# Performance work log

Measured on AMD Instinct MI355X. Metric: run time of the kernel, lower is better.

## Reference

```python
import jax, jax.numpy as jnp
import numpy as np

SEQ, B, N = 128, 64, 128
IN_DIM, HID = 64, 128
K = 2          # max_diffusion_step
L = 2          # num_rnn_layers
M = K + 1      # num_matrices = n_supports*K + 1 (one 'laplacian' support)


def setup_inputs() -> dict:
    key = jax.random.key(0)
    ks = jax.random.split(key, 8)
    inputs = jax.random.normal(ks[0], (SEQ, B, N, IN_DIM), jnp.float32)
    initial_hidden_state = jnp.zeros((L, B, N * HID), jnp.float32)
    # scaled normalized-laplacian-like support; 1/N keeps chebyshev terms bounded
    supports = jax.random.normal(ks[1], (1, N, N), jnp.float32) / N

    def w(k, fan_in, out):
        return jax.random.normal(k, (fan_in, out), jnp.float32) / np.sqrt(fan_in).astype(np.float32)

    in0 = M * (IN_DIM + HID)   # layer 0 gconv input features (576)
    in1 = M * (HID + HID)      # layer 1 gconv input features (768)
    return {
        "inputs": inputs,
        "initial_hidden_state": initial_hidden_state,
        "supports": supports,
        "Wg0": w(ks[2], in0, 2 * HID), "bg0": jnp.zeros((2 * HID,), jnp.float32),
        "Wc0": w(ks[3], in0, HID),     "bc0": jnp.zeros((HID,), jnp.float32),
        "Wg1": w(ks[4], in1, 2 * HID), "bg1": jnp.zeros((2 * HID,), jnp.float32),
        "Wc1": w(ks[5], in1, HID),     "bc1": jnp.zeros((HID,), jnp.float32),
    }


def _gconv(x, support, W, b):
    # x: (B, N, F). Chebyshev diffusion: x0, x1=S@x0, x_k=2*S@x_{k-1}-x_{k-2}
    x0 = x
    x1 = jnp.einsum('mn,bnf->bmf', support, x0)
    mats = [x0, x1]
    for _ in range(2, K + 1):
        x2 = 2.0 * jnp.einsum('mn,bnf->bmf', support, x1) - x0
        mats.append(x2)
        x0, x1 = x1, x2
    xs = jnp.stack(mats, axis=-1)                 # (B, N, F, M) -- torch layout
    xs = xs.reshape(x.shape[0], x.shape[1], -1)   # (B, N, F*M)
    return xs @ W + b                             # (B, N, out)


def _dcgru_layer(x_seq, h0, support, Wg, bg, Wc, bc):
    # x_seq: (T, B, N, F); h0: (B, N, HID)
    def step(h, x_t):
        cat = jnp.concatenate([x_t, h], axis=-1)
        gates = jax.nn.sigmoid(_gconv(cat, support, Wg, bg))
        r, u = jnp.split(gates, 2, axis=-1)
        c = jnp.tanh(_gconv(jnp.concatenate([x_t, r * h], axis=-1), support, Wc, bc))
        h_new = u * h + (1.0 - u) * c
        return h_new, h_new
    return jax.lax.scan(step, h0, x_seq)


def reference(inputs, initial_hidden_state, supports, Wg0, bg0, Wc0, bc0, Wg1, bg1, Wc1, bc1):
    sup = supports[0]
    h0_0 = initial_hidden_state[0].reshape(B, N, HID)
    h0_1 = initial_hidden_state[1].reshape(B, N, HID)
    h_last0, ys0 = _dcgru_layer(inputs, h0_0, sup, Wg0, bg0, Wc0, bc0)
    h_last1, ys1 = _dcgru_layer(ys0, h0_1, sup, Wg1, bg1, Wc1, bc1)
    output_hidden = jnp.stack([h_last0, h_last1], axis=0).reshape(L, B, N * HID)
    outputs = ys1.reshape(SEQ, B, N * HID)
    return output_hidden, outputs
```

## Files before the change

kernel.cpp:

```cpp
#include <hip/hip_runtime.h>
#include <math.h>

#define SEQ 128
#define B 64
#define NN 128
#define IN_DIM 64
#define HID 128
#define BNH (B*NN*HID)

typedef unsigned short u16;
typedef __bf16 bf16x8 __attribute__((ext_vector_type(8)));
typedef float f32x4 __attribute__((ext_vector_type(4)));

__device__ __forceinline__ u16 f2bf(float f) {
    union { float f; unsigned u; } x; x.f = f;
    unsigned r = x.u + 0x7fffu + ((x.u >> 16) & 1u);
    return (u16)(r >> 16);
}
__device__ __forceinline__ float bf2f(u16 b) {
    union { unsigned u; float f; } x; x.u = ((unsigned)b) << 16; return x.f;
}
__device__ __forceinline__ bf16x8 ld_frag(const u16* p) {
    union { uint4 q; bf16x8 v; } u;
    u.q = *(const uint4*)p;
    return u.v;
}
__device__ __forceinline__ uint2 pack4(const f32x4& a) {
    uint2 pk;
    pk.x = (unsigned)f2bf(a[0]) | ((unsigned)f2bf(a[1]) << 16);
    pk.y = (unsigned)f2bf(a[2]) | ((unsigned)f2bf(a[3]) << 16);
    return pk;
}
__device__ __forceinline__ bf16x8 cvt8(const float* p) {
    float4 v0 = *(const float4*)p, v1 = *(const float4*)(p + 4);
    union { uint4 q; bf16x8 v; } t;
    t.q.x = (unsigned)f2bf(v0.x) | ((unsigned)f2bf(v0.y) << 16);
    t.q.y = (unsigned)f2bf(v0.z) | ((unsigned)f2bf(v0.w) << 16);
    t.q.z = (unsigned)f2bf(v1.x) | ((unsigned)f2bf(v1.y) << 16);
    t.q.w = (unsigned)f2bf(v1.z) | ((unsigned)f2bf(v1.w) << 16);
    return t.v;
}

__global__ void prep_A2_kernel(const float* __restrict__ S, u16* __restrict__ A2bf) {
    int idx = blockIdx.x * 256 + threadIdx.x;
    int m = idx >> 7, n = idx & 127;
    A2bf[idx] = f2bf(S[idx]);
    float acc = 0.f;
    #pragma unroll 4
    for (int k = 0; k < 128; ++k) acc += S[m*128 + k] * S[k*128 + n];
    A2bf[16384 + idx] = f2bf(2.f*acc - (m == n ? 1.f : 0.f));
}

__global__ void prep_A2f_kernel(const u16* __restrict__ A2bf, u16* __restrict__ A2f) {
    int idx = blockIdx.x * 256 + threadIdx.x;
    int j = idx & 7, lane = (idx >> 3) & 63, g = (idx >> 9) & 15, kc = idx >> 13;
    int mp = g*16 + (lane & 15);
    int n  = kc*32 + (lane >> 4)*8 + j;
    A2f[idx] = A2bf[mp*128 + n];
}

__global__ void prep_WTf_kernel(const float* __restrict__ W, u16* __restrict__ WTf,
                                int F, int NO) {
    int KK = 3 * F;
    int idx = blockIdx.x * 256 + threadIdx.x;
    if (idx >= NO * KK) return;
    int per = 512 * (NO/16);
    int kc = idx / per, rem = idx % per;
    int cg = rem >> 9, lane = (rem >> 3) & 63, j = idx & 7;
    int col = cg*16 + (lane & 15);
    int k = kc*32 + (lane >> 4)*8 + j;
    int m = k / F, f = k - m*F;
    WTf[idx] = f2bf(W[(size_t)(f*3 + m) * NO + col]);
}

__global__ void init_h_kernel(const float* __restrict__ h,
                              u16* __restrict__ hbf0, u16* __restrict__ h0T,
                              u16* __restrict__ hbf1, u16* __restrict__ h1T) {
    int i = blockIdx.x * 256 + threadIdx.x;
    int which = (i >= BNH);
    int j = which ? i - BNH : i;
    u16 v = f2bf(h[i]);
    int bn = j >> 7, col = j & 127;
    if (!which) { hbf0[j] = v; h0T[(size_t)col*8192 + bn] = v; }
    else        { hbf1[j] = v; h1T[(size_t)col*8192 + bn] = v; }
}

template<int L>
__device__ __forceinline__ void stepA(
    int b, int nh, int mh,
    const float* __restrict__ xf, const u16* __restrict__ hbX, const u16* __restrict__ xT,
    const u16* __restrict__ hbH, const u16* __restrict__ hTH,
    const u16* __restrict__ A2f, const u16* __restrict__ WTg, const float* __restrict__ bg,
    u16* __restrict__ rhb, u16* __restrict__ rhbT, float* __restrict__ ub,
    u16* __restrict__ xsgF, u16* smem)
{
    constexpr int FIN = L ? 128 : 64;
    constexpr int F   = L ? 256 : 192;
    constexpr int KK  = 3 * F;
    constexpr int FH  = F / 2;
    constexpr int NF2 = F / 32;
    const int tid = threadIdx.x;
    const int lane = tid & 63, w = tid >> 6;
    const int l15 = lane & 15, l16 = lane >> 4;

    if (L == 0) {
        for (int task = tid; task < 1024; task += 256) {
            int ng8 = task & 15, f = task >> 4, n0 = ng8*8, bn = b*NN + n0;
            union { uint4 q; u16 s[8]; } t;
            #pragma unroll
            for (int i = 0; i < 8; ++i) t.s[i] = f2bf(xf[(size_t)(bn + i)*IN_DIM + f]);
            *(uint4*)&smem[f*128 + (n0 ^ ((f & 7)*8))] = t.q;
        }
    }
    {
        const int R0 = L ? 0 : 64;
        const int NT = (F - R0) * 16;
        for (int task = tid; task < NT; task += 256) {
            int ng8 = task & 15, f = R0 + (task >> 4);
            const u16* src;
            if (L == 1) src = (f < 128) ? (xT + (size_t)f*8192) : (hTH + (size_t)(f - 128)*8192);
            else        src = hTH + (size_t)(f - 64)*8192;
            uint4 q = *(const uint4*)(src + (size_t)b*128 + ng8*8);
            *(uint4*)&smem[f*128 + ((ng8*8) ^ ((f & 7)*8))] = q;
        }
    }
    __syncthreads();

    const int mq = w;
    #pragma unroll
    for (int p = 0; p < 2; ++p) {
        const int fbase = (p == 0) ? FH : 0;
        f32x4 dacc[NF2][2];
        #pragma unroll
        for (int ff = 0; ff < NF2; ++ff)
            #pragma unroll
            for (int mm = 0; mm < 2; ++mm) dacc[ff][mm] = (f32x4)(0.f);
        #pragma unroll
        for (int kc = 0; kc < 4; ++kc) {
            bf16x8 bfr[2];
            #pragma unroll
            for (int mm = 0; mm < 2; ++mm) {
                const int g = (mq >> 1)*8 + mh*4 + (mq & 1)*2 + mm;
                bfr[mm] = ld_frag(A2f + (((size_t)kc*16 + g)*64 + lane)*8);
            }
            #pragma unroll
            for (int ff = 0; ff < NF2; ++ff) {
                const int f = fbase + ff*16 + l15;
                bf16x8 afr = ld_frag(&smem[f*128 + ((kc*32 + l16*8) ^ ((f & 7)*8))]);
                #pragma unroll
                for (int mm = 0; mm < 2; ++mm)
                    dacc[ff][mm] = __builtin_amdgcn_mfma_f32_16x16x32_bf16(afr, bfr[mm], dacc[ff][mm], 0, 0, 0);
            }
        }
        __syncthreads();
        const int fh = (p == 0) ? 1 : 0;
        #pragma unroll
        for (int ff = 0; ff < NF2; ++ff) {
            const int f4 = fbase + ff*16 + l16*4;
            const int col = f4 - fbase;
            #pragma unroll
            for (int mm = 0; mm < 2; ++mm) {
                const int r = mq*32 + mm*16 + l15;
                uint2 pk = pack4(dacc[ff][mm]);
                *(uint2*)&smem[fh*16384 + r*128 + (col ^ ((r & 7)*8))] = pk;
                if (nh == 0 && f4 < FIN) {
                    const int slot = r >> 6, node = mh*64 + (r & 63);
                    size_t off = ((((size_t)b*2 + slot)*(FIN/32) + (f4 >> 5))*8 + (node >> 4))*512
                               + (((f4 >> 3) & 3)*16 + (node & 15))*8 + (f4 & 7);
                    *(uint2*)(xsgF + off) = pk;
                }
            }
        }
    }
    __syncthreads();

    f32x4 pacc[4][2];
    #pragma unroll
    for (int fi = 0; fi < 4; ++fi)
        #pragma unroll
        for (int gj = 0; gj < 2; ++gj) pacc[fi][gj] = (f32x4)(0.f);

    #pragma unroll
    for (int kc = 0; kc < KK/32; ++kc) {
        const int k = kc*32, m = k / F, fIn = k - m*F;
        bf16x8 bb[2];
        #pragma unroll
        for (int gj = 0; gj < 2; ++gj) {
            const int cg = nh*8 + w*2 + gj;
            bb[gj] = ld_frag(WTg + (((size_t)kc*16 + cg)*64 + lane)*8);
        }
        #pragma unroll
        for (int fi = 0; fi < 4; ++fi) {
            const int node = mh*64 + fi*16 + l15;
            const int bn = b*NN + node;
            bf16x8 a;
            if (m == 0) {
                if (fIn < FIN) {
                    if (L == 0) a = cvt8(xf + (size_t)bn*IN_DIM + fIn + l16*8);
                    else        a = ld_frag(hbX + (size_t)bn*HID + fIn + l16*8);
                } else a = ld_frag(hbH + (size_t)bn*HID + (fIn - FIN) + l16*8);
            } else {
                const int r = (m - 1)*64 + fi*16 + l15;
                const int fh = (fIn >= FH) ? 1 : 0;
                const int col = fIn - fh*FH + l16*8;
                a = ld_frag(&smem[fh*16384 + r*128 + (col ^ ((r & 7)*8))]);
            }
            #pragma unroll
            for (int gj = 0; gj < 2; ++gj)
                pacc[fi][gj] = __builtin_amdgcn_mfma_f32_16x16x32_bf16(a, bb[gj], pacc[fi][gj], 0, 0, 0);
        }
    }
    #pragma unroll
    for (int fi = 0; fi < 4; ++fi) {
        const int node0 = mh*64 + fi*16 + l16*4;
        #pragma unroll
        for (int gj = 0; gj < 2; ++gj) {
            const int cl = (w*2 + gj)*16 + l15;
            if (nh == 0) {
                const float bcv = bg[cl];
                union { uint2 q; u16 s[4]; } pk;
                #pragma unroll
                for (int rr = 0; rr < 4; ++rr) {
                    const int bn = b*NN + node0 + rr;
                    const float v = pacc[fi][gj][rr] + bcv;
                    const float s = 1.f/(1.f + expf(-v));
                    const u16 rv = f2bf(s * bf2f(hbH[(size_t)bn*HID + cl]));
                    pk.s[rr] = rv;
                    rhb[(size_t)bn*HID + cl] = rv;
                }
                *(uint2*)&rhbT[(size_t)cl*8192 + (size_t)b*128 + node0] = pk.q;
            } else {
                const float bcv = bg[128 + cl];
                #pragma unroll
                for (int rr = 0; rr < 4; ++rr) {
                    const int bn = b*NN + node0 + rr;
                    const float v = pacc[fi][gj][rr] + bcv;
                    ub[(size_t)bn*HID + cl] = 1.f/(1.f + expf(-v));
                }
            }
        }
    }
}

template<int L>
__device__ __forceinline__ void stepB(
    int b, int mh,
    const float* __restrict__ xf, const u16* __restrict__ hbX,
    const u16* __restrict__ rhb, const u16* __restrict__ rhbT, const float* __restrict__ ub,
    const u16* __restrict__ xsgF, const u16* __restrict__ A2f,
    const u16* __restrict__ WTc, const float* __restrict__ bc,
    const float* __restrict__ hfR, float* __restrict__ hfW,
    u16* __restrict__ hbfW, u16* __restrict__ hTW,
    float* __restrict__ out2, u16* smem )
{
    constexpr int FIN = L ? 128 : 64;
    constexpr int F   = L ? 256 : 192;
    constexpr int KK  = 3 * F;
    const int tid = threadIdx.x;
    const int lane = tid & 63, w = tid >> 6;
    const int l15 = lane & 15, l16 = lane >> 4;

    f32x4 d2[4][2];
    #pragma unroll
    for (int ff = 0; ff < 4; ++ff)
        #pragma unroll
        for (int mm = 0; mm < 2; ++mm) d2[ff][mm] = (f32x4)(0.f);
    #pragma unroll
    for (int kc = 0; kc < 4; ++kc) {
        bf16x8 bfr[2];
        #pragma unroll
        for (int mm = 0; mm < 2; ++mm) {
            const int g = (w & 1)*8 + mh*2 + mm;
            bfr[mm] = ld_frag(A2f + (((size_t)kc*16 + g)*64 + lane)*8);
        }
        #pragma unroll
        for (int ff = 0; ff < 4; ++ff) {
            const int c = (w >> 1)*64 + ff*16 + l15;
            bf16x8 afr = ld_frag(rhbT + (size_t)c*8192 + (size_t)b*128 + kc*32 + l16*8);
            #pragma unroll
            for (int mm = 0; mm < 2; ++mm)
                d2[ff][mm] = __builtin_amdgcn_mfma_f32_16x16x32_bf16(afr, bfr[mm], d2[ff][mm], 0, 0, 0);
        }
    }
    #pragma unroll
    for (int ff = 0; ff < 4; ++ff) {
        const int c4 = (w >> 1)*64 + ff*16 + l16*4;
        #pragma unroll
        for (int mm = 0; mm < 2; ++mm) {
            const int r2 = (w & 1)*32 + mm*16 + l15;
            *(uint2*)&smem[r2*128 + (c4 ^ ((r2 & 7)*8))] = pack4(d2[ff][mm]);
        }
    }
    __syncthreads();

    f32x4 cacc[2][2];
    #pragma unroll
    for (int fi = 0; fi < 2; ++fi)
        #pragma unroll
        for (int gj = 0; gj < 2; ++gj) cacc[fi][gj] = (f32x4)(0.f);

    #pragma unroll
    for (int kc = 0; kc < KK/32; ++kc) {
        const int k = kc*32, m = k / F, fIn = k - m*F;
        bf16x8 bb[2];
        #pragma unroll
        for (int gj = 0; gj < 2; ++gj)
            bb[gj] = ld_frag(WTc + (((size_t)kc*8 + w*2 + gj)*64 + lane)*8);
        #pragma unroll
        for (int fi = 0; fi < 2; ++fi) {
            const int node = mh*32 + fi*16 + l15;
            const int bn = b*NN + node;
            bf16x8 a;
            if (m == 0) {
                if (fIn < FIN) {
                    if (L == 0) a = cvt8(xf + (size_t)bn*IN_DIM + fIn + l16*8);
                    else        a = ld_frag(hbX + (size_t)bn*HID + fIn + l16*8);
                } else a = ld_frag(rhb + (size_t)bn*HID + (fIn - FIN) + l16*8);
            } else if (fIn < FIN) {
                size_t off = ((((size_t)b*2 + (m - 1))*(FIN/32) + (fIn >> 5))*8 + (mh*2 + fi))*512
                           + (size_t)lane*8;
                a = ld_frag(xsgF + off);
            } else {
                const int r2 = (m - 1)*32 + fi*16 + l15;
                const int col = fIn - FIN + l16*8;
                a = ld_frag(&smem[r2*128 + (col ^ ((r2 & 7)*8))]);
            }
            #pragma unroll
            for (int gj = 0; gj < 2; ++gj)
                cacc[fi][gj] = __builtin_amdgcn_mfma_f32_16x16x32_bf16(a, bb[gj], cacc[fi][gj], 0, 0, 0);
        }
    }
    #pragma unroll
    for (int fi = 0; fi < 2; ++fi) {
        const int node0 = mh*32 + fi*16 + l16*4;
        #pragma unroll
        for (int gj = 0; gj < 2; ++gj) {
            const int cl = (w*2 + gj)*16 + l15;
            const float bcv = bc[cl];
            union { uint2 q; u16 s[4]; } pk;
            #pragma unroll
            for (int rr = 0; rr < 4; ++rr) {
                const int bn = b*NN + node0 + rr;
                const float v = cacc[fi][gj][rr] + bcv;
                const float cnd = tanhf(v);
                const float uu = ub[(size_t)bn*HID + cl];
                const float ho = hfR[(size_t)bn*HID + cl];
                const float hn = uu*ho + (1.f - uu)*cnd;
                hfW[(size_t)bn*HID + cl] = hn;
                const u16 hv = f2bf(hn);
                hbfW[(size_t)bn*HID + cl] = hv;
                pk.s[rr] = hv;
                if (L == 1) out2[(size_t)bn*HID + cl] = hn;
            }
            *(uint2*)&hTW[(size_t)cl*8192 + (size_t)b*128 + node0] = pk.q;
        }
    }
}

__global__ __launch_bounds__(256, 2) void kA(int zoff,
    const float* xf, const u16* A2f,
    const u16* hbf0r, const u16* h0Tr, const u16* hbf1r, const u16* h1Tr,
    const u16* WTgf0, const float* bg0, u16* rhb0, u16* rhbT0, float* ub0, u16* xsgF0,
    const u16* WTgf1, const float* bg1, u16* rhb1, u16* rhbT1, float* ub1, u16* xsgF1)
{
    extern __shared__ u16 smem[];
    const int b = blockIdx.x, nh = blockIdx.y >> 1, mh = blockIdx.y & 1;
    if ((int)blockIdx.z + zoff == 0)
        stepA<0>(b, nh, mh, xf, nullptr, nullptr, hbf0r, h0Tr, A2f,
                 WTgf0, bg0, rhb0, rhbT0, ub0, xsgF0, smem);
    else
        stepA<1>(b, nh, mh, nullptr, hbf0r, h0Tr, hbf1r, h1Tr, A2f,
                 WTgf1, bg1, rhb1, rhbT1, ub1, xsgF1, smem);
}

__global__ __launch_bounds__(256, 2) void kB(int zoff,
    const float* xf, const u16* A2f, const u16* hbf0r,
    const u16* rhb0, const u16* rhbT0, const float* ub0, const u16* xsgF0,
    const u16* WTcf0, const float* bc0,
    const float* hf0r, float* hf0w, u16* hbf0w, u16* h0Tw,
    const u16* rhb1, const u16* rhbT1, const float* ub1, const u16* xsgF1,
    const u16* WTcf1, const float* bc1,
    const float* hf1r, float* hf1w, u16* hbf1w, u16* h1Tw,
    float* out2)
{
    extern __shared__ u16 smem[];
    const int b = blockIdx.x, mh = blockIdx.y;
    if ((int)blockIdx.z + zoff == 0)
        stepB<0>(b, mh, xf, nullptr, rhb0, rhbT0, ub0, xsgF0, A2f, WTcf0, bc0,
                 hf0r, hf0w, hbf0w, h0Tw, nullptr, smem);
    else
        stepB<1>(b, mh, nullptr, hbf0r, rhb1, rhbT1, ub1, xsgF1, A2f, WTcf1, bc1,
                 hf1r, hf1w, hbf1w, h1Tw, out2, smem);
}

extern "C" void kernel_launch(void* const* d_in, const int* in_sizes, int n_in,
                              void* d_out, int out_size, void* d_ws, size_t ws_size,
                              hipStream_t stream) {
    (void)in_sizes; (void)n_in; (void)out_size; (void)ws_size;
    const float* inputs = (const float*)d_in[0];
    const float* h_init = (const float*)d_in[1];
    const float* S      = (const float*)d_in[2];
    const float* Wg0 = (const float*)d_in[3];
    const float* bg0 = (const float*)d_in[4];
    const float* Wc0 = (const float*)d_in[5];
    const float* bc0 = (const float*)d_in[6];
    const float* Wg1 = (const float*)d_in[7];
    const float* bg1 = (const float*)d_in[8];
    const float* Wc1 = (const float*)d_in[9];
    const float* bc1 = (const float*)d_in[10];

    float* out = (float*)d_out;
    float* outputs = out + 2 * (size_t)BNH;

    char* ws = (char*)d_ws;
    u16* A2bf  = (u16*)ws;                      ws += 32768 * 2;
    u16* A2f   = (u16*)ws;                      ws += 32768 * 2;
    u16* WTgf0 = (u16*)ws;                      ws += 256*576 * 2;
    u16* WTcf0 = (u16*)ws;                      ws += 128*576 * 2;
    u16* WTgf1 = (u16*)ws;                      ws += 256*768 * 2;
    u16* WTcf1 = (u16*)ws;                      ws += 128*768 * 2;
    ws = (char*)(((size_t)ws + 255) & ~(size_t)255);
    u16* xsgF0 = (u16*)ws;                      ws += (size_t)64*2*2*4096 * 2;
    u16* xsgF1 = (u16*)ws;                      ws += (size_t)64*2*4*4096 * 2;
    u16* rhb0  = (u16*)ws;                      ws += (size_t)BNH * 2;
    u16* rhb1  = (u16*)ws;                      ws += (size_t)BNH * 2;
    u16* rhbT0 = (u16*)ws;                      ws += (size_t)BNH * 2;
    u16* rhbT1 = (u16*)ws;                      ws += (size_t)BNH * 2;
    float* ub0 = (float*)ws;                    ws += (size_t)BNH * 4;
    float* ub1 = (float*)ws;                    ws += (size_t)BNH * 4;
    float* hf0_[2]; u16* hbf0_[2]; u16* h0T_[2];
    float* hf1_[2]; u16* hbf1_[2]; u16* h1T_[2];
    for (int i = 0; i < 2; ++i) {
        hf0_[i]  = (float*)ws;                  ws += (size_t)BNH * 4;
        hf1_[i]  = (float*)ws;                  ws += (size_t)BNH * 4;
        hbf0_[i] = (u16*)ws;                    ws += (size_t)BNH * 2;
        hbf1_[i] = (u16*)ws;                    ws += (size_t)BNH * 2;
        h0T_[i]  = (u16*)ws;                    ws += (size_t)BNH * 2;
        h1T_[i]  = (u16*)ws;                    ws += (size_t)BNH * 2;
    }

    hipFuncSetAttribute((const void*)kA, hipFuncAttributeMaxDynamicSharedMemorySize, 65536);
    hipFuncSetAttribute((const void*)kB, hipFuncAttributeMaxDynamicSharedMemorySize, 16384);

    hipMemcpyAsync(hf0_[1], h_init, (size_t)BNH * sizeof(float), hipMemcpyDeviceToDevice, stream);
    hipMemcpyAsync(hf1_[0], h_init + BNH, (size_t)BNH * sizeof(float), hipMemcpyDeviceToDevice, stream);
    init_h_kernel<<<(2*BNH + 255)/256, 256, 0, stream>>>(h_init, hbf0_[1], h0T_[1], hbf1_[0], h1T_[0]);
    prep_A2_kernel<<<64, 256, 0, stream>>>(S, A2bf);
    prep_A2f_kernel<<<128, 256, 0, stream>>>(A2bf, A2f);
    prep_WTf_kernel<<<(256*576 + 255)/256, 256, 0, stream>>>(Wg0, WTgf0, 192, 256);
    prep_WTf_kernel<<<(128*576 + 255)/256, 256, 0, stream>>>(Wc0, WTcf0, 192, 128);
    prep_WTf_kernel<<<(256*768 + 255)/256, 256, 0, stream>>>(Wg1, WTgf1, 256, 256);
    prep_WTf_kernel<<<(128*768 + 255)/256, 256, 0, stream>>>(Wc1, WTcf1, 256, 128);

    for (int tau = 0; tau <= SEQ; ++tau) {
        const int nz = (tau == 0 || tau == SEQ) ? 1 : 2;
        const int zoff = (tau == SEQ) ? 1 : 0;
        const int rb = (tau + 1) & 1, wb = tau & 1;
        const int tx = (tau < SEQ) ? tau : (SEQ - 1);
        const float* xt = inputs + (size_t)tx * B * NN * IN_DIM;
        float* out2 = outputs + (size_t)((tau > 0) ? tau - 1 : 0) * BNH;

        kA<<<dim3(64, 4, nz), 256, 65536, stream>>>(zoff,
            xt, A2f,
            hbf0_[rb], h0T_[rb], hbf1_[rb], h1T_[rb],
            WTgf0, bg0, rhb0, rhbT0, ub0, xsgF0,
            WTgf1, bg1, rhb1, rhbT1, ub1, xsgF1);
        kB<<<dim3(64, 4, nz), 256, 16384, stream>>>(zoff,
            xt, A2f, hbf0_[rb],
            rhb0, rhbT0, ub0, xsgF0, WTcf0, bc0,
            hf0_[rb], hf0_[wb], hbf0_[wb], h0T_[wb],
            rhb1, rhbT1, ub1, xsgF1, WTcf1, bc1,
            hf1_[rb], hf1_[wb], hbf1_[wb], h1T_[wb],
            out2);
    }
    hipMemcpyAsync(out, hf0_[1], (size_t)BNH * sizeof(float), hipMemcpyDeviceToDevice, stream);
    hipMemcpyAsync(out + BNH, hf1_[0], (size_t)BNH * sizeof(float), hipMemcpyDeviceToDevice, stream);
}
```

Measured before the change: 7.870 ms.

## Replace per-step kernel launches with persistent kernel and per-batch atomic barriers

The 258 small kernel launches (kA/kB per timestep) are replaced by a single persistent kernel of 512 blocks. Each batch element's 8 blocks (4 per layer) synchronise through a spin barrier on an atomic counter in global memory, and the barrier counter is zeroed in init_h_kernel. This removes launch overhead and grid-wide drains between stages, letting different batches progress independently. It relies on all 512 blocks being co-resident (2 per CU with 64KB LDS each) and risks deadlock or spin contention if that does not hold.

```diff
diff --git a/kernel.cpp b/kernel.cpp
--- a/kernel.cpp
+++ b/kernel.cpp
@@ -75,8 +75,10 @@
 
 __global__ void init_h_kernel(const float* __restrict__ h,
                               u16* __restrict__ hbf0, u16* __restrict__ h0T,
-                              u16* __restrict__ hbf1, u16* __restrict__ h1T) {
+                              u16* __restrict__ hbf1, u16* __restrict__ h1T,
+                              unsigned* __restrict__ bar) {
     int i = blockIdx.x * 256 + threadIdx.x;
+    if (blockIdx.x == 0 && threadIdx.x < 64) bar[threadIdx.x * 16] = 0;
     int which = (i >= BNH);
     int j = which ? i - BNH : i;
     u16 v = f2bf(h[i]);
@@ -357,40 +359,84 @@
     }
 }
 
-__global__ __launch_bounds__(256, 2) void kA(int zoff,
-    const float* xf, const u16* A2f,
-    const u16* hbf0r, const u16* h0Tr, const u16* hbf1r, const u16* h1Tr,
-    const u16* WTgf0, const float* bg0, u16* rhb0, u16* rhbT0, float* ub0, u16* xsgF0,
-    const u16* WTgf1, const float* bg1, u16* rhb1, u16* rhbT1, float* ub1, u16* xsgF1)
-{
+struct P {
+    const float* inputs; float* outputs;
+    const u16 *A2f, *WTg0, *WTc0, *WTg1, *WTc1;
+    const float *bg0, *bc0, *bg1, *bc1;
+    u16 *rhb0, *rhb1, *rhbT0, *rhbT1;
+    float *ub0, *ub1;
+    u16 *xsgF0, *xsgF1;
+    float *hf0_0, *hf0_1, *hf1_0, *hf1_1;
+    u16 *hbf0_0, *hbf0_1, *hbf1_0, *hbf1_1;
+    u16 *h0T_0, *h0T_1, *h1T_0, *h1T_1;
+    unsigned* bar;
+};
+
+__device__ __forceinline__ void bbar(unsigned* barw, unsigned tgt) {
+    __syncthreads();
+    if (threadIdx.x == 0) {
+        __hip_atomic_fetch_add(barw, 1u, __ATOMIC_RELEASE, __HIP_MEMORY_SCOPE_AGENT);
+        while (__hip_atomic_load(barw, __ATOMIC_ACQUIRE, __HIP_MEMORY_SCOPE_AGENT) < tgt)
+            __builtin_amdgcn_s_sleep(2);
+    }
+    __syncthreads();
+}
+
+template<int L>
+__device__ void run_chain(const P& p, int b, int quad, u16* smem) {
+    unsigned* barw = p.bar + b*16;
+    unsigned tgt = 0;
+    const int nh = quad >> 1, mh = quad & 1;
+    for (int iter = 0; iter <= SEQ; ++iter) {
+        const int rb = (iter + 1) & 1, wb = iter & 1;
+        const bool act = (L == 0) ? (iter < SEQ) : (iter >= 1);
+        const float* xf = p.inputs + (size_t)iter * (B*NN*IN_DIM);
+        const u16* hbf0r = rb ? p.hbf0_1 : p.hbf0_0;
+        const u16* h0Tr  = rb ? p.h0T_1  : p.h0T_0;
+
+        if (act) {
+            if (L == 0) {
+                stepA<0>(b, nh, mh, xf, nullptr, nullptr, hbf0r, h0Tr, p.A2f,
+                         p.WTg0, p.bg0, p.rhb0, p.rhbT0, p.ub0, p.xsgF0, smem);
+            } else {
+                const u16* hbf1r = rb ? p.hbf1_1 : p.hbf1_0;
+                const u16* h1Tr  = rb ? p.h1T_1  : p.h1T_0;
+                stepA<1>(b, nh, mh, nullptr, hbf0r, h0Tr, hbf1r, h1Tr, p.A2f,
+                         p.WTg1, p.bg1, p.rhb1, p.rhbT1, p.ub1, p.xsgF1, smem);
+            }
+        }
+        tgt += 8; bbar(barw, tgt);
+
+        if (act) {
+            if (L == 0) {
+                const float* hf0r = rb ? p.hf0_1 : p.hf0_0;
+                float* hf0w = wb ? p.hf0_1 : p.hf0_0;
+                u16* hbf0w = wb ? p.hbf0_1 : p.hbf0_0;
+                u16* h0Tw  = wb ? p.h0T_1  : p.h0T_0;
+                stepB<0>(b, quad, xf, nullptr, p.rhb0, p.rhbT0, p.ub0, p.xsgF0, p.A2f,
+                         p.WTc0, p.bc0, hf0r, hf0w, hbf0w, h0Tw, nullptr, smem);
+            } else {
+                const float* hf1r = rb ? p.hf1_1 : p.hf1_0;
+                float* hf1w = wb ? p.hf1_1 : p.hf1_0;
+                u16* hbf1w = wb ? p.hbf1_1 : p.hbf1_0;
+                u16* h1Tw  = wb ? p.h1T_1  : p.h1T_0;
+                float* out2 = p.outputs + (size_t)(iter - 1) * BNH;
+                stepB<1>(b, quad, nullptr, hbf0r, p.rhb1, p.rhbT1, p.ub1, p.xsgF1, p.A2f,
+                         p.WTc1, p.bc1, hf1r, hf1w, hbf1w, h1Tw, out2, smem);
+            }
+        }
+        tgt += 8; bbar(barw, tgt);
+    }
+}
+
+__global__ __launch_bounds__(256, 2) void kPersist(P p) {
     extern __shared__ u16 smem[];
-    const int b = blockIdx.x, nh = blockIdx.y >> 1, mh = blockIdx.y & 1;
-    if ((int)blockIdx.z + zoff == 0)
-        stepA<0>(b, nh, mh, xf, nullptr, nullptr, hbf0r, h0Tr, A2f,
-                 WTgf0, bg0, rhb0, rhbT0, ub0, xsgF0, smem);
-    else
-        stepA<1>(b, nh, mh, nullptr, hbf0r, h0Tr, hbf1r, h1Tr, A2f,
-                 WTgf1, bg1, rhb1, rhbT1, ub1, xsgF1, smem);
-}
-
-__global__ __launch_bounds__(256, 2) void kB(int zoff,
-    const float* xf, const u16* A2f, const u16* hbf0r,
-    const u16* rhb0, const u16* rhbT0, const float* ub0, const u16* xsgF0,
-    const u16* WTcf0, const float* bc0,
-    const float* hf0r, float* hf0w, u16* hbf0w, u16* h0Tw,
-    const u16* rhb1, const u16* rhbT1, const float* ub1, const u16* xsgF1,
-    const u16* WTcf1, const float* bc1,
-    const float* hf1r, float* hf1w, u16* hbf1w, u16* h1Tw,
-    float* out2)
-{
-    extern __shared__ u16 smem[];
-    const int b = blockIdx.x, mh = blockIdx.y;
-    if ((int)blockIdx.z + zoff == 0)
-        stepB<0>(b, mh, xf, nullptr, rhb0, rhbT0, ub0, xsgF0, A2f, WTcf0, bc0,
-                 hf0r, hf0w, hbf0w, h0Tw, nullptr, smem);
-    else
-        stepB<1>(b, mh, nullptr, hbf0r, rhb1, rhbT1, ub1, xsgF1, A2f, WTcf1, bc1,
-                 hf1r, hf1w, hbf1w, h1Tw, out2, smem);
+    const int bid = blockIdx.x;
+    const int b = bid & 63;
+    const int sub = bid >> 6;
+    const int L = sub >> 2, quad = sub & 3;
+    if (L == 0) run_chain<0>(p, b, quad, smem);
+    else        run_chain<1>(p, b, quad, smem);
 }
 
 extern "C" void kernel_launch(void* const* d_in, const int* in_sizes, int n_in,
@@ -419,6 +465,8 @@
     u16* WTcf0 = (u16*)ws;                      ws += 128*576 * 2;
     u16* WTgf1 = (u16*)ws;                      ws += 256*768 * 2;
     u16* WTcf1 = (u16*)ws;                      ws += 128*768 * 2;
+    ws = (char*)(((size_t)ws + 255) & ~(size_t)255);
+    unsigned* bar = (unsigned*)ws;              ws += 64*16*4;
     ws = (char*)(((size_t)ws + 255) & ~(size_t)255);
     u16* xsgF0 = (u16*)ws;                      ws += (size_t)64*2*2*4096 * 2;
     u16* xsgF1 = (u16*)ws;                      ws += (size_t)64*2*4*4096 * 2;
@@ -439,12 +487,11 @@
         h1T_[i]  = (u16*)ws;                    ws += (size_t)BNH * 2;
     }
 
-    hipFuncSetAttribute((const void*)kA, hipFuncAttributeMaxDynamicSharedMemorySize, 65536);
-    hipFuncSetAttribute((const void*)kB, hipFuncAttributeMaxDynamicSharedMemorySize, 16384);
+    hipFuncSetAttribute((const void*)kPersist, hipFuncAttributeMaxDynamicSharedMemorySize, 65536);
 
     hipMemcpyAsync(hf0_[1], h_init, (size_t)BNH * sizeof(float), hipMemcpyDeviceToDevice, stream);
     hipMemcpyAsync(hf1_[0], h_init + BNH, (size_t)BNH * sizeof(float), hipMemcpyDeviceToDevice, stream);
-    init_h_kernel<<<(2*BNH + 255)/256, 256, 0, stream>>>(h_init, hbf0_[1], h0T_[1], hbf1_[0], h1T_[0]);
+    init_h_kernel<<<(2*BNH + 255)/256, 256, 0, stream>>>(h_init, hbf0_[1], h0T_[1], hbf1_[0], h1T_[0], bar);
     prep_A2_kernel<<<64, 256, 0, stream>>>(S, A2bf);
     prep_A2f_kernel<<<128, 256, 0, stream>>>(A2bf, A2f);
     prep_WTf_kernel<<<(256*576 + 255)/256, 256, 0, stream>>>(Wg0, WTgf0, 192, 256);
@@ -452,27 +499,19 @@
     prep_WTf_kernel<<<(256*768 + 255)/256, 256, 0, stream>>>(Wg1, WTgf1, 256, 256);
     prep_WTf_kernel<<<(128*768 + 255)/256, 256, 0, stream>>>(Wc1, WTcf1, 256, 128);
 
-    for (int tau = 0; tau <= SEQ; ++tau) {
-        const int nz = (tau == 0 || tau == SEQ) ? 1 : 2;
-        const int zoff = (tau == SEQ) ? 1 : 0;
-        const int rb = (tau + 1) & 1, wb = tau & 1;
-        const int tx = (tau < SEQ) ? tau : (SEQ - 1);
-        const float* xt = inputs + (size_t)tx * B * NN * IN_DIM;
-        float* out2 = outputs + (size_t)((tau > 0) ? tau - 1 : 0) * BNH;
-
-        kA<<<dim3(64, 4, nz), 256, 65536, stream>>>(zoff,
-            xt, A2f,
-            hbf0_[rb], h0T_[rb], hbf1_[rb], h1T_[rb],
-            WTgf0, bg0, rhb0, rhbT0, ub0, xsgF0,
-            WTgf1, bg1, rhb1, rhbT1, ub1, xsgF1);
-        kB<<<dim3(64, 4, nz), 256, 16384, stream>>>(zoff,
-            xt, A2f, hbf0_[rb],
-            rhb0, rhbT0, ub0, xsgF0, WTcf0, bc0,
-            hf0_[rb], hf0_[wb], hbf0_[wb], h0T_[wb],
-            rhb1, rhbT1, ub1, xsgF1, WTcf1, bc1,
-            hf1_[rb], hf1_[wb], hbf1_[wb], h1T_[wb],
-            out2);
-    }
+    P p;
+    p.inputs = inputs; p.outputs = outputs;
+    p.A2f = A2f; p.WTg0 = WTgf0; p.WTc0 = WTcf0; p.WTg1 = WTgf1; p.WTc1 = WTcf1;
+    p.bg0 = bg0; p.bc0 = bc0; p.bg1 = bg1; p.bc1 = bc1;
+    p.rhb0 = rhb0; p.rhb1 = rhb1; p.rhbT0 = rhbT0; p.rhbT1 = rhbT1;
+    p.ub0 = ub0; p.ub1 = ub1; p.xsgF0 = xsgF0; p.xsgF1 = xsgF1;
+    p.hf0_0 = hf0_[0]; p.hf0_1 = hf0_[1]; p.hf1_0 = hf1_[0]; p.hf1_1 = hf1_[1];
+    p.hbf0_0 = hbf0_[0]; p.hbf0_1 = hbf0_[1]; p.hbf1_0 = hbf1_[0]; p.hbf1_1 = hbf1_[1];
+    p.h0T_0 = h0T_[0]; p.h0T_1 = h0T_[1]; p.h1T_0 = h1T_[0]; p.h1T_1 = h1T_[1];
+    p.bar = bar;
+
+    kPersist<<<512, 256, 65536, stream>>>(p);
+
     hipMemcpyAsync(out, hf0_[1], (size_t)BNH * sizeof(float), hipMemcpyDeviceToDevice, stream);
     hipMemcpyAsync(out + BNH, hf1_[0], (size_t)BNH * sizeof(float), hipMemcpyDeviceToDevice, stream);
 }
```

Measured after the change: 30.27 ms. 3.85x slower.

## Split DCGRU step kernels over finer node tiles and stage diffusion via global

Applied to the files above, without the earlier changes.

Both step kernels now launch 64x8 blocks instead of 64x4, and each block handles fewer nodes. Launch bounds move from 2 to 4 blocks per SM to raise occupancy. The shared-memory staging of inputs and hidden state in the gate kernel is removed: a one-time kernel pre-transposes all timesteps of the input to bf16, and diffusion results go to global scratch buffers that are read back after a block barrier. This removes large shared-memory use and boosts parallelism. The cost is duplicated diffusion work across nh blocks, extra global and L2 traffic, and a sizable extra workspace buffer.

```diff
diff --git a/kernel.cpp b/kernel.cpp
--- a/kernel.cpp
+++ b/kernel.cpp
@@ -73,6 +73,21 @@
     WTf[idx] = f2bf(W[(size_t)(f*3 + m) * NO + col]);
 }
 
+__global__ void prep_xT_kernel(const float* __restrict__ x, u16* __restrict__ xT) {
+    __shared__ u16 tile[64][72];
+    const int t = blockIdx.y, n0 = blockIdx.x * 64;
+    const int tid = threadIdx.x;
+    for (int i = tid; i < 4096; i += 256) {
+        int row = i >> 6, f = i & 63;
+        tile[f][row] = f2bf(x[((size_t)t*8192 + n0 + row)*64 + f]);
+    }
+    __syncthreads();
+    for (int i = tid; i < 4096; i += 256) {
+        int f = i >> 6, col = i & 63;
+        xT[((size_t)t*64 + f)*8192 + n0 + col] = tile[f][col];
+    }
+}
+
 __global__ void init_h_kernel(const float* __restrict__ h,
                               u16* __restrict__ hbf0, u16* __restrict__ h0T,
                               u16* __restrict__ hbf1, u16* __restrict__ h1T) {
@@ -88,11 +103,14 @@
 template<int L>
 __device__ __forceinline__ void stepA(
     int b, int nh, int mh,
-    const float* __restrict__ xf, const u16* __restrict__ hbX, const u16* __restrict__ xT,
-    const u16* __restrict__ hbH, const u16* __restrict__ hTH,
+    const float* __restrict__ xf,
+    const u16* __restrict__ xTt,
+    const u16* __restrict__ hbX,
+    const u16* __restrict__ hbH,
+    const u16* __restrict__ hTH,
     const u16* __restrict__ A2f, const u16* __restrict__ WTg, const float* __restrict__ bg,
     u16* __restrict__ rhb, u16* __restrict__ rhbT, float* __restrict__ ub,
-    u16* __restrict__ xsgF, u16* smem)
+    u16* __restrict__ Dg)
 {
     constexpr int FIN = L ? 128 : 64;
     constexpr int F   = L ? 256 : 192;
@@ -103,80 +121,44 @@
     const int lane = tid & 63, w = tid >> 6;
     const int l15 = lane & 15, l16 = lane >> 4;
 
-    if (L == 0) {
-        for (int task = tid; task < 1024; task += 256) {
-            int ng8 = task & 15, f = task >> 4, n0 = ng8*8, bn = b*NN + n0;
-            union { uint4 q; u16 s[8]; } t;
-            #pragma unroll
-            for (int i = 0; i < 8; ++i) t.s[i] = f2bf(xf[(size_t)(bn + i)*IN_DIM + f]);
-            *(uint4*)&smem[f*128 + (n0 ^ ((f & 7)*8))] = t.q;
-        }
-    }
-    {
-        const int R0 = L ? 0 : 64;
-        const int NT = (F - R0) * 16;
-        for (int task = tid; task < NT; task += 256) {
-            int ng8 = task & 15, f = R0 + (task >> 4);
-            const u16* src;
-            if (L == 1) src = (f < 128) ? (xT + (size_t)f*8192) : (hTH + (size_t)(f - 128)*8192);
-            else        src = hTH + (size_t)(f - 64)*8192;
-            uint4 q = *(const uint4*)(src + (size_t)b*128 + ng8*8);
-            *(uint4*)&smem[f*128 + ((ng8*8) ^ ((f & 7)*8))] = q;
-        }
-    }
-    __syncthreads();
-
-    const int mq = w;
+    const int g     = (w >> 1)*8 + mh*2 + (w & 1);
+    const int slot  = w >> 1;
+    const int nodeg = mh*2 + (w & 1);
     #pragma unroll
     for (int p = 0; p < 2; ++p) {
-        const int fbase = (p == 0) ? FH : 0;
-        f32x4 dacc[NF2][2];
-        #pragma unroll
-        for (int ff = 0; ff < NF2; ++ff)
-            #pragma unroll
-            for (int mm = 0; mm < 2; ++mm) dacc[ff][mm] = (f32x4)(0.f);
+        const int fbase = p ? FH : 0;
+        f32x4 dacc[NF2];
+        #pragma unroll
+        for (int ff = 0; ff < NF2; ++ff) dacc[ff] = (f32x4)(0.f);
         #pragma unroll
         for (int kc = 0; kc < 4; ++kc) {
-            bf16x8 bfr[2];
-            #pragma unroll
-            for (int mm = 0; mm < 2; ++mm) {
-                const int g = (mq >> 1)*8 + mh*4 + (mq & 1)*2 + mm;
-                bfr[mm] = ld_frag(A2f + (((size_t)kc*16 + g)*64 + lane)*8);
-            }
+            bf16x8 bfr = ld_frag(A2f + (((size_t)kc*16 + g)*64 + lane)*8);
             #pragma unroll
             for (int ff = 0; ff < NF2; ++ff) {
-                const int f = fbase + ff*16 + l15;
-                bf16x8 afr = ld_frag(&smem[f*128 + ((kc*32 + l16*8) ^ ((f & 7)*8))]);
-                #pragma unroll
-                for (int mm = 0; mm < 2; ++mm)
-                    dacc[ff][mm] = __builtin_amdgcn_mfma_f32_16x16x32_bf16(afr, bfr[mm], dacc[ff][mm], 0, 0, 0);
+                const int fr = fbase + ff*16;
+                const int f  = fr + l15;
+                const u16* src;
+                if (L == 1) src = (fr < 128) ? (xTt + (size_t)f*8192)
+                                             : (hTH + (size_t)(f - 128)*8192);
+                else        src = (fr < 64)  ? (xTt + (size_t)f*8192)
+                                             : (hTH + (size_t)(f - 64)*8192);
+                bf16x8 afr = ld_frag(src + (size_t)b*128 + kc*32 + l16*8);
+                dacc[ff] = __builtin_amdgcn_mfma_f32_16x16x32_bf16(afr, bfr, dacc[ff], 0, 0, 0);
             }
         }
-        __syncthreads();
-        const int fh = (p == 0) ? 1 : 0;
         #pragma unroll
         for (int ff = 0; ff < NF2; ++ff) {
             const int f4 = fbase + ff*16 + l16*4;
-            const int col = f4 - fbase;
-            #pragma unroll
-            for (int mm = 0; mm < 2; ++mm) {
-                const int r = mq*32 + mm*16 + l15;
-                uint2 pk = pack4(dacc[ff][mm]);
-                *(uint2*)&smem[fh*16384 + r*128 + (col ^ ((r & 7)*8))] = pk;
-                if (nh == 0 && f4 < FIN) {
-                    const int slot = r >> 6, node = mh*64 + (r & 63);
-                    size_t off = ((((size_t)b*2 + slot)*(FIN/32) + (f4 >> 5))*8 + (node >> 4))*512
-                               + (((f4 >> 3) & 3)*16 + (node & 15))*8 + (f4 & 7);
-                    *(uint2*)(xsgF + off) = pk;
-                }
-            }
+            size_t off = (((size_t)(b*2 + slot)*(F/32) + (f4 >> 5))*8 + nodeg)*512
+                       + (((f4 >> 3) & 3)*16 + l15)*8 + (f4 & 7);
+            *(uint2*)(Dg + off) = pack4(dacc[ff]);
         }
     }
     __syncthreads();
 
-    f32x4 pacc[4][2];
-    #pragma unroll
-    for (int fi = 0; fi < 4; ++fi)
+    f32x4 pacc[2][2];
+    #pragma unroll
+    for (int fi = 0; fi < 2; ++fi)
         #pragma unroll
         for (int gj = 0; gj < 2; ++gj) pacc[fi][gj] = (f32x4)(0.f);
 
@@ -190,8 +172,8 @@
             bb[gj] = ld_frag(WTg + (((size_t)kc*16 + cg)*64 + lane)*8);
         }
         #pragma unroll
-        for (int fi = 0; fi < 4; ++fi) {
-            const int node = mh*64 + fi*16 + l15;
+        for (int fi = 0; fi < 2; ++fi) {
+            const int node = mh*32 + fi*16 + l15;
             const int bn = b*NN + node;
             bf16x8 a;
             if (m == 0) {
@@ -200,10 +182,9 @@
                     else        a = ld_frag(hbX + (size_t)bn*HID + fIn + l16*8);
                 } else a = ld_frag(hbH + (size_t)bn*HID + (fIn - FIN) + l16*8);
             } else {
-                const int r = (m - 1)*64 + fi*16 + l15;
-                const int fh = (fIn >= FH) ? 1 : 0;
-                const int col = fIn - fh*FH + l16*8;
-                a = ld_frag(&smem[fh*16384 + r*128 + (col ^ ((r & 7)*8))]);
+                size_t off = (((size_t)(b*2 + (m-1))*(F/32) + (fIn >> 5))*8 + (mh*2 + fi))*512
+                           + (size_t)lane*8;
+                a = ld_frag(Dg + off);
             }
             #pragma unroll
             for (int gj = 0; gj < 2; ++gj)
@@ -211,8 +192,8 @@
         }
     }
     #pragma unroll
-    for (int fi = 0; fi < 4; ++fi) {
-        const int node0 = mh*64 + fi*16 + l16*4;
+    for (int fi = 0; fi < 2; ++fi) {
+        const int node0 = mh*32 + fi*16 + l16*4;
         #pragma unroll
         for (int gj = 0; gj < 2; ++gj) {
             const int cl = (w*2 + gj)*16 + l15;
@@ -247,7 +228,7 @@
     int b, int mh,
     const float* __restrict__ xf, const u16* __restrict__ hbX,
     const u16* __restrict__ rhb, const u16* __restrict__ rhbT, const float* __restrict__ ub,
-    const u16* __restrict__ xsgF, const u16* __restrict__ A2f,
+    const u16* __restrict__ Dg0, const u16* __restrict__ A2f,
     const u16* __restrict__ WTc, const float* __restrict__ bc,
     const float* __restrict__ hfR, float* __restrict__ hfW,
     u16* __restrict__ hbfW, u16* __restrict__ hTW,
@@ -260,44 +241,40 @@
     const int lane = tid & 63, w = tid >> 6;
     const int l15 = lane & 15, l16 = lane >> 4;
 
-    f32x4 d2[4][2];
-    #pragma unroll
-    for (int ff = 0; ff < 4; ++ff)
-        #pragma unroll
-        for (int mm = 0; mm < 2; ++mm) d2[ff][mm] = (f32x4)(0.f);
+    f32x4 d2[2][2];
+    #pragma unroll
+    for (int cc = 0; cc < 2; ++cc)
+        #pragma unroll
+        for (int mm = 0; mm < 2; ++mm) d2[cc][mm] = (f32x4)(0.f);
     #pragma unroll
     for (int kc = 0; kc < 4; ++kc) {
         bf16x8 bfr[2];
         #pragma unroll
-        for (int mm = 0; mm < 2; ++mm) {
-            const int g = (w & 1)*8 + mh*2 + mm;
-            bfr[mm] = ld_frag(A2f + (((size_t)kc*16 + g)*64 + lane)*8);
-        }
-        #pragma unroll
-        for (int ff = 0; ff < 4; ++ff) {
-            const int c = (w >> 1)*64 + ff*16 + l15;
+        for (int mm = 0; mm < 2; ++mm)
+            bfr[mm] = ld_frag(A2f + (((size_t)kc*16 + mm*8 + mh)*64 + lane)*8);
+        #pragma unroll
+        for (int cc = 0; cc < 2; ++cc) {
+            const int c = (w*2 + cc)*16 + l15;
             bf16x8 afr = ld_frag(rhbT + (size_t)c*8192 + (size_t)b*128 + kc*32 + l16*8);
             #pragma unroll
             for (int mm = 0; mm < 2; ++mm)
-                d2[ff][mm] = __builtin_amdgcn_mfma_f32_16x16x32_bf16(afr, bfr[mm], d2[ff][mm], 0, 0, 0);
-        }
-    }
-    #pragma unroll
-    for (int ff = 0; ff < 4; ++ff) {
-        const int c4 = (w >> 1)*64 + ff*16 + l16*4;
+                d2[cc][mm] = __builtin_amdgcn_mfma_f32_16x16x32_bf16(afr, bfr[mm], d2[cc][mm], 0, 0, 0);
+        }
+    }
+    #pragma unroll
+    for (int cc = 0; cc < 2; ++cc) {
+        const int c4 = (w*2 + cc)*16 + l16*4;
         #pragma unroll
         for (int mm = 0; mm < 2; ++mm) {
-            const int r2 = (w & 1)*32 + mm*16 + l15;
-            *(uint2*)&smem[r2*128 + (c4 ^ ((r2 & 7)*8))] = pack4(d2[ff][mm]);
+            const int r2 = mm*16 + l15;
+            *(uint2*)&smem[r2*128 + (c4 ^ ((r2 & 7)*8))] = pack4(d2[cc][mm]);
         }
     }
     __syncthreads();
 
-    f32x4 cacc[2][2];
-    #pragma unroll
-    for (int fi = 0; fi < 2; ++fi)
-        #pragma unroll
-        for (int gj = 0; gj < 2; ++gj) cacc[fi][gj] = (f32x4)(0.f);
+    f32x4 cacc[2];
+    #pragma unroll
+    for (int gj = 0; gj < 2; ++gj) cacc[gj] = (f32x4)(0.f);
 
     #pragma unroll
     for (int kc = 0; kc < KK/32; ++kc) {
@@ -306,90 +283,83 @@
         #pragma unroll
         for (int gj = 0; gj < 2; ++gj)
             bb[gj] = ld_frag(WTc + (((size_t)kc*8 + w*2 + gj)*64 + lane)*8);
-        #pragma unroll
-        for (int fi = 0; fi < 2; ++fi) {
-            const int node = mh*32 + fi*16 + l15;
-            const int bn = b*NN + node;
-            bf16x8 a;
-            if (m == 0) {
-                if (fIn < FIN) {
-                    if (L == 0) a = cvt8(xf + (size_t)bn*IN_DIM + fIn + l16*8);
-                    else        a = ld_frag(hbX + (size_t)bn*HID + fIn + l16*8);
-                } else a = ld_frag(rhb + (size_t)bn*HID + (fIn - FIN) + l16*8);
-            } else if (fIn < FIN) {
-                size_t off = ((((size_t)b*2 + (m - 1))*(FIN/32) + (fIn >> 5))*8 + (mh*2 + fi))*512
-                           + (size_t)lane*8;
-                a = ld_frag(xsgF + off);
-            } else {
-                const int r2 = (m - 1)*32 + fi*16 + l15;
-                const int col = fIn - FIN + l16*8;
-                a = ld_frag(&smem[r2*128 + (col ^ ((r2 & 7)*8))]);
-            }
-            #pragma unroll
-            for (int gj = 0; gj < 2; ++gj)
-                cacc[fi][gj] = __builtin_amdgcn_mfma_f32_16x16x32_bf16(a, bb[gj], cacc[fi][gj], 0, 0, 0);
-        }
-    }
-    #pragma unroll
-    for (int fi = 0; fi < 2; ++fi) {
-        const int node0 = mh*32 + fi*16 + l16*4;
-        #pragma unroll
-        for (int gj = 0; gj < 2; ++gj) {
-            const int cl = (w*2 + gj)*16 + l15;
-            const float bcv = bc[cl];
-            union { uint2 q; u16 s[4]; } pk;
-            #pragma unroll
-            for (int rr = 0; rr < 4; ++rr) {
-                const int bn = b*NN + node0 + rr;
-                const float v = cacc[fi][gj][rr] + bcv;
-                const float cnd = tanhf(v);
-                const float uu = ub[(size_t)bn*HID + cl];
-                const float ho = hfR[(size_t)bn*HID + cl];
-                const float hn = uu*ho + (1.f - uu)*cnd;
-                hfW[(size_t)bn*HID + cl] = hn;
-                const u16 hv = f2bf(hn);
-                hbfW[(size_t)bn*HID + cl] = hv;
-                pk.s[rr] = hv;
-                if (L == 1) out2[(size_t)bn*HID + cl] = hn;
-            }
-            *(uint2*)&hTW[(size_t)cl*8192 + (size_t)b*128 + node0] = pk.q;
-        }
-    }
-}
-
-__global__ __launch_bounds__(256, 2) void kA(int zoff,
-    const float* xf, const u16* A2f,
+        const int node = mh*16 + l15;
+        const int bn = b*NN + node;
+        bf16x8 a;
+        if (m == 0) {
+            if (fIn < FIN) {
+                if (L == 0) a = cvt8(xf + (size_t)bn*IN_DIM + fIn + l16*8);
+                else        a = ld_frag(hbX + (size_t)bn*HID + fIn + l16*8);
+            } else a = ld_frag(rhb + (size_t)bn*HID + (fIn - FIN) + l16*8);
+        } else if (fIn < FIN) {
+            size_t off = (((size_t)(b*2 + (m-1))*(F/32) + (fIn >> 5))*8 + mh)*512
+                       + (size_t)lane*8;
+            a = ld_frag(Dg0 + off);
+        } else {
+            const int r2 = (m-1)*16 + l15;
+            a = ld_frag(&smem[r2*128 + (((fIn - FIN) + l16*8) ^ ((r2 & 7)*8))]);
+        }
+        #pragma unroll
+        for (int gj = 0; gj < 2; ++gj)
+            cacc[gj] = __builtin_amdgcn_mfma_f32_16x16x32_bf16(a, bb[gj], cacc[gj], 0, 0, 0);
+    }
+    const int node0 = mh*16 + l16*4;
+    #pragma unroll
+    for (int gj = 0; gj < 2; ++gj) {
+        const int cl = (w*2 + gj)*16 + l15;
+        const float bcv = bc[cl];
+        union { uint2 q; u16 s[4]; } pk;
+        #pragma unroll
+        for (int rr = 0; rr < 4; ++rr) {
+            const int bn = b*NN + node0 + rr;
+            const float v = cacc[gj][rr] + bcv;
+            const float cnd = tanhf(v);
+            const float uu = ub[(size_t)bn*HID + cl];
+            const float ho = hfR[(size_t)bn*HID + cl];
+            const float hn = uu*ho + (1.f - uu)*cnd;
+            hfW[(size_t)bn*HID + cl] = hn;
+            const u16 hv = f2bf(hn);
+            hbfW[(size_t)bn*HID + cl] = hv;
+            pk.s[rr] = hv;
+            if (L == 1) out2[(size_t)bn*HID + cl] = hn;
+        }
+        *(uint2*)&hTW[(size_t)cl*8192 + (size_t)b*128 + node0] = pk.q;
+    }
+}
+
+__global__ __launch_bounds__(256, 4) void kA(int zoff,
+    const float* xf, const u16* xTt, const u16* A2f,
     const u16* hbf0r, const u16* h0Tr, const u16* hbf1r, const u16* h1Tr,
-    const u16* WTgf0, const float* bg0, u16* rhb0, u16* rhbT0, float* ub0, u16* xsgF0,
-    const u16* WTgf1, const float* bg1, u16* rhb1, u16* rhbT1, float* ub1, u16* xsgF1)
+    const u16* WTgf0, const float* bg0, u16* rhb0, u16* rhbT0, float* ub0, u16* Dg00, u16* Dg01,
+    const u16* WTgf1, const float* bg1, u16* rhb1, u16* rhbT1, float* ub1, u16* Dg10, u16* Dg11)
 {
-    extern __shared__ u16 smem[];
-    const int b = blockIdx.x, nh = blockIdx.y >> 1, mh = blockIdx.y & 1;
+    const int b = blockIdx.x, y = blockIdx.y;
+    const int nh = y >> 2, mh = y & 3;
     if ((int)blockIdx.z + zoff == 0)
-        stepA<0>(b, nh, mh, xf, nullptr, nullptr, hbf0r, h0Tr, A2f,
-                 WTgf0, bg0, rhb0, rhbT0, ub0, xsgF0, smem);
+        stepA<0>(b, nh, mh, xf, xTt, nullptr, hbf0r, h0Tr, A2f, WTgf0, bg0,
+                 rhb0, rhbT0, ub0, nh ? Dg01 : Dg00);
     else
-        stepA<1>(b, nh, mh, nullptr, hbf0r, h0Tr, hbf1r, h1Tr, A2f,
-                 WTgf1, bg1, rhb1, rhbT1, ub1, xsgF1, smem);
-}
-
-__global__ __launch_bounds__(256, 2) void kB(int zoff,
+        stepA<1>(b, nh, mh, nullptr, h0Tr, hbf0r, hbf1r, h1Tr, A2f, WTgf1, bg1,
+                 rhb1, rhbT1, ub1, nh ? Dg11 : Dg10);
+}
+
+__global__ __launch_bounds__(256, 4) void kB(int zoff,
     const float* xf, const u16* A2f, const u16* hbf0r,
-    const u16* rhb0, const u16* rhbT0, const float* ub0, const u16* xsgF0,
+    const u16* rhb0, const u16* rhbT0, const float* ub0, const u16* Dg00,
     const u16* WTcf0, const float* bc0,
     const float* hf0r, float* hf0w, u16* hbf0w, u16* h0Tw,
-    const u16* rhb1, const u16* rhbT1, const float* ub1, const u16* xsgF1,
+    const u16* rhb1, const u16* rhbT1, const float* ub1, const u16* Dg10,
     const u16* WTcf1, const float* bc1,
     const float* hf1r, float* hf1w, u16* hbf1w, u16* h1Tw,
     float* out2)
 {
-    extern __shared__ u16 smem[];
+    __shared__ u16 smem[32*128];
     const int b = blockIdx.x, mh = blockIdx.y;
     if ((int)blockIdx.z + zoff == 0)
-        stepB<0>(b, mh, xf, nullptr, rhb0, rhbT0, ub0, xsgF0, A2f, WTcf0, bc0,
+        stepB<0>(b, mh, xf, nullptr, rhb0, rhbT0, ub0, Dg00, A2f, WTcf0, bc0,
                  hf0r, hf0w, hbf0w, h0Tw, nullptr, smem);
     else
-        stepB<1>(b, mh, nullptr, hbf0r, rhb1, rhbT1, ub1, xsgF1, A2f, WTcf1, bc1,
+        stepB<1>(b, mh, nullptr, hbf0r, rhb1, rhbT1, ub1, Dg10, A2f, WTcf1, bc1,
                  hf1r, hf1w, hbf1w, h1Tw, out2, smem);
 }
 
@@ -420,8 +390,11 @@
     u16* WTgf1 = (u16*)ws;                      ws += 256*768 * 2;
     u16* WTcf1 = (u16*)ws;                      ws += 128*768 * 2;
     ws = (char*)(((size_t)ws + 255) & ~(size_t)255);
-    u16* xsgF0 = (u16*)ws;                      ws += (size_t)64*2*2*4096 * 2;
-    u16* xsgF1 = (u16*)ws;                      ws += (size_t)64*2*4*4096 * 2;
+    u16* xTall = (u16*)ws;                      ws += (size_t)SEQ*64*8192 * 2;
+    u16* Dg00  = (u16*)ws;                      ws += (size_t)128*6*8*512 * 2;
+    u16* Dg01  = (u16*)ws;                      ws += (size_t)128*6*8*512 * 2;
+    u16* Dg10  = (u16*)ws;                      ws += (size_t)128*8*8*512 * 2;
+    u16* Dg11  = (u16*)ws;                      ws += (size_t)128*8*8*512 * 2;
     u16* rhb0  = (u16*)ws;                      ws += (size_t)BNH * 2;
     u16* rhb1  = (u16*)ws;                      ws += (size_t)BNH * 2;
     u16* rhbT0 = (u16*)ws;                      ws += (size_t)BNH * 2;
@@ -439,9 +412,6 @@
         h1T_[i]  = (u16*)ws;                    ws += (size_t)BNH * 2;
     }
 
-    hipFuncSetAttribute((const void*)kA, hipFuncAttributeMaxDynamicSharedMemorySize, 65536);
-    hipFuncSetAttribute((const void*)kB, hipFuncAttributeMaxDynamicSharedMemorySize, 16384);
-
     hipMemcpyAsync(hf0_[1], h_init, (size_t)BNH * sizeof(float), hipMemcpyDeviceToDevice, stream);
     hipMemcpyAsync(hf1_[0], h_init + BNH, (size_t)BNH * sizeof(float), hipMemcpyDeviceToDevice, stream);
     init_h_kernel<<<(2*BNH + 255)/256, 256, 0, stream>>>(h_init, hbf0_[1], h0T_[1], hbf1_[0], h1T_[0]);
@@ -451,6 +421,7 @@
     prep_WTf_kernel<<<(128*576 + 255)/256, 256, 0, stream>>>(Wc0, WTcf0, 192, 128);
     prep_WTf_kernel<<<(256*768 + 255)/256, 256, 0, stream>>>(Wg1, WTgf1, 256, 256);
     prep_WTf_kernel<<<(128*768 + 255)/256, 256, 0, stream>>>(Wc1, WTcf1, 256, 128);
+    prep_xT_kernel<<<dim3(128, SEQ), 256, 0, stream>>>(inputs, xTall);
 
     for (int tau = 0; tau <= SEQ; ++tau) {
         const int nz = (tau == 0 || tau == SEQ) ? 1 : 2;
@@ -458,18 +429,19 @@
         const int rb = (tau + 1) & 1, wb = tau & 1;
         const int tx = (tau < SEQ) ? tau : (SEQ - 1);
         const float* xt = inputs + (size_t)tx * B * NN * IN_DIM;
+        const u16* xTt = xTall + (size_t)tx * 64 * 8192;
         float* out2 = outputs + (size_t)((tau > 0) ? tau - 1 : 0) * BNH;
 
-        kA<<<dim3(64, 4, nz), 256, 65536, stream>>>(zoff,
-            xt, A2f,
+        kA<<<dim3(64, 8, nz), 256, 0, stream>>>(zoff,
+            xt, xTt, A2f,
             hbf0_[rb], h0T_[rb], hbf1_[rb], h1T_[rb],
-            WTgf0, bg0, rhb0, rhbT0, ub0, xsgF0,
-            WTgf1, bg1, rhb1, rhbT1, ub1, xsgF1);
-        kB<<<dim3(64, 4, nz), 256, 16384, stream>>>(zoff,
+            WTgf0, bg0, rhb0, rhbT0, ub0, Dg00, Dg01,
+            WTgf1, bg1, rhb1, rhbT1, ub1, Dg10, Dg11);
+        kB<<<dim3(64, 8, nz), 256, 0, stream>>>(zoff,
             xt, A2f, hbf0_[rb],
-            rhb0, rhbT0, ub0, xsgF0, WTcf0, bc0,
+            rhb0, rhbT0, ub0, Dg00, WTcf0, bc0,
             hf0_[rb], hf0_[wb], hbf0_[wb], h0T_[wb],
-            rhb1, rhbT1, ub1, xsgF1, WTcf1, bc1,
+            rhb1, rhbT1, ub1, Dg10, WTcf1, bc1,
             hf1_[rb], hf1_[wb], hbf1_[wb], h1T_[wb],
             out2);
     }
```

After: 9.751 ms. +23.9%, slower.
